# Optimization experiments

Hardware: AMD Instinct MI355X
Metric: run time of the kernel (lower is better)

The kernel has to match this reference:

```python
import jax, jax.numpy as jnp
import numpy as np

T = 64      # simulation_length
B = 128     # batch
D = 2048    # flattened input dim / axons per core
N = 2048    # neurons per core
L = 4       # number of cores (chain, latency = index)
OUT = 1024  # number of output_sources


def setup_inputs() -> dict:
    key = jax.random.key(0)
    k0, k1, k2, k3 = jax.random.split(key, 4)
    x = jax.random.uniform(k0, (B, D), dtype=jnp.float32)          # rate-coded input in [0,1)
    # core_params[l] = core_matrix.transpose() -> shape [N, A]; scaled for sane membrane dynamics
    W = jax.random.normal(k1, (L, N, D), dtype=jnp.float32) * 0.05
    thresholds = jnp.ones((L,), dtype=jnp.float32)
    # axon_sources: per-core irregular gather indices into previous core's neurons (input for l=0)
    axon_idx = jax.random.randint(k2, (L, D), 0, D, dtype=jnp.int32)
    out_idx = jax.random.randint(k3, (OUT,), 0, N, dtype=jnp.int32)
    return dict(x=x, W=W, thresholds=thresholds, axon_idx=axon_idx,
                out_idx=out_idx, simulation_length=T)


def _ideal_spike_scan(avg, thr, T):
    """Per-cycle: m += avg; spike = (m > thr); m[m > thr] -= thr.  avg: [B, N]."""
    def step(m, _):
        m = m + avg
        s = (m > thr).astype(m.dtype)
        return m - thr * s, s
    _, spikes = jax.lax.scan(step, jnp.zeros_like(avg), None, length=T)
    return spikes  # [T, B, N]


def reference(x, W, thresholds, axon_idx, out_idx, simulation_length):
    T = simulation_length
    L = W.shape[0]
    # generate_input_spike_train: x replicated across all cycles -> cache[-1]
    prev = jnp.broadcast_to(x, (T,) + x.shape)  # [T, B, D]
    for l in range(L):
        # get_signal_tensor: gather axon source signals for every cycle
        gathered = prev[:, :, axon_idx[l]]                    # [T, B, A]
        # per-cycle matmul: torch.matmul(core_params, sig.T).T == sig @ W[l].T
        val = jnp.einsum('tba,na->tbn', gathered, W[l])       # [T, B, N]
        avg = val.mean(axis=0)                                # avg_values [B, N]
        # ideal membrane integrate + threshold-reset recurrence -> out spike train
        prev = _ideal_spike_scan(avg, thresholds[l], T)       # [T, B, N]
    # output_signals: sum of output-source spikes over all cycles
    return prev[:, :, out_idx].sum(axis=0)                    # [B, OUT]
```

## Files before the change

kernel.cpp:

```cpp
#include <hip/hip_runtime.h>

#define BB   128
#define DD   2048
#define NN   2048
#define LL   4
#define OUTN 1024
#define JBQ  32
#define NDIG 5

#define NWDIG 12288
#define NG0   1024
#define NCSR  4

typedef double double4v __attribute__((ext_vector_type(4)));
typedef int    int4v    __attribute__((ext_vector_type(4)));
typedef char   char4v   __attribute__((ext_vector_type(4)));

__global__ __launch_bounds__(256) void prep_kernel(
    const float* __restrict__ W1,
    const float* __restrict__ x,
    const int*   __restrict__ axon,
    const int*   __restrict__ oidx,
    signed char* __restrict__ Wd,
    float*       __restrict__ At,
    int*         __restrict__ off,
    int*         __restrict__ lst)
{
    __shared__ int hist[2048];
    __shared__ int part[256];

    const int t  = threadIdx.x;
    const int bk = blockIdx.x;
    const size_t DP = (size_t)NN * DD;

    if (bk < NWDIG) {
        size_t i  = (size_t)bk * 256 + t;
        int    l  = (int)(i / (DP / 4));
        size_t e4 = i - (size_t)l * (DP / 4);
        int n = (int)(e4 >> 9);
        int k = (int)(e4 & 511) * 4;
        float4 w = *(const float4*)(W1 + (size_t)l * DP + (size_t)n * DD + k);
        const float wv[4] = {w.x, w.y, w.z, w.w};
        unsigned long long V[4];
        #pragma unroll
        for (int e = 0; e < 4; ++e)
            V[e] = (unsigned long long)(__double2ll_rn((double)wv[e] * 0x1p33)
                                        + (1LL << 34));
        signed char* base = Wd + (size_t)l * 5 * DP
                          + (size_t)(n >> 5) * 65536 + (size_t)(k >> 6) * 2048
                          + (n & 31) * 64 + (k & 63);
        #pragma unroll
        for (int j = 0; j < NDIG; ++j) {
            char4v p = { (char)((V[0] >> (7 * j)) & 127),
                         (char)((V[1] >> (7 * j)) & 127),
                         (char)((V[2] >> (7 * j)) & 127),
                         (char)((V[3] >> (7 * j)) & 127) };
            *(char4v*)(base + (size_t)j * DP) = p;
        }
        return;
    }
    if (bk < NWDIG + NG0) {
        int i = (bk - NWDIG) * 256 + t;
        int b = i >> 11;
        int k = i & (DD - 1);
        At[(size_t)(k >> 6) * 8192 + b * 64 + (k & 63)] = x[b * DD + axon[k]];
        return;
    }
    {
        const int m   = bk - (NWDIG + NG0);
        const int* ip = (m < 3) ? (axon + (size_t)(m + 1) * DD) : oidx;
        const int cnt = (m < 3) ? DD : OUTN;
        int* offG = off + m * 2052;
        int* lstG = lst + m * 2048;

        for (int i = t; i < 2048; i += 256) hist[i] = 0;
        __syncthreads();
        for (int e = t; e < cnt; e += 256) atomicAdd(&hist[ip[e]], 1);
        __syncthreads();

        const int b0 = t * 8;
        int s = 0;
        #pragma unroll
        for (int i = 0; i < 8; ++i) s += hist[b0 + i];
        part[t] = s;
        __syncthreads();
        for (int d = 1; d < 256; d <<= 1) {
            int v = (t >= d) ? part[t - d] : 0;
            __syncthreads();
            part[t] += v;
            __syncthreads();
        }
        int base = part[t] - s;
        #pragma unroll
        for (int i = 0; i < 8; ++i) {
            int h = hist[b0 + i];
            offG[b0 + i] = base;
            hist[b0 + i] = base;
            base += h;
        }
        if (t == 255) offG[2048] = base;
        __syncthreads();
        for (int e = t; e < cnt; e += 256) {
            int n = ip[e];
            int pos = atomicAdd(&hist[n], 1);
            lstG[pos] = e;
        }
    }
}

__global__ __launch_bounds__(256, 4) void layer0_kernel(
    const float* __restrict__ Atile,
    const float* __restrict__ Wl,
    const float* __restrict__ thr,
    const int*   __restrict__ Tptr,
    const int* __restrict__ goff, const int* __restrict__ glst,
    signed char* __restrict__ g8n)
{
    __shared__ double red[4 * 64 * 4];

    const int t    = threadIdx.x;
    const int wq   = t >> 6;
    const int lane = t & 63;
    const int q    = lane >> 4;
    const int c    = lane & 15;

    const int g     = blockIdx.x;
    const int btile = (g >> 3) & 7;
    const int nsup  = (g & 7) | ((g >> 6) << 3);
    const int n0    = nsup * 16;
    const int bcol  = btile * 16 + c;

    double4v pr = {0., 0., 0., 0.}, pcv = {0., 0., 0., 0.};
    pr  = __builtin_amdgcn_mfma_f64_16x16x4f64(0.25 * (double)c, 1.0, pr, 0, 0, 0);
    pcv = __builtin_amdgcn_mfma_f64_16x16x4f64(0.25, (double)c, pcv, 0, 0, 0);
    int rowD[4], colD[4];
    #pragma unroll
    for (int r = 0; r < 4; ++r) {
        rowD[r] = (int)(pr[r] + 0.25);
        colD[r] = (int)(pcv[r] + 0.25);
    }

    double4v acc[4] = {{0.,0.,0.,0.},{0.,0.,0.,0.},{0.,0.,0.,0.},{0.,0.,0.,0.}};

    const int    kbase = wq * (DD / 4);
    const float* wb0   = Wl + (size_t)(n0 + c) * DD + kbase + 4 * q;

    float4 wv0[4], sv[4];
    #pragma unroll
    for (int p = 0; p < 4; ++p) wv0[p] = *(const float4*)(wb0 + 16 * p);
    #pragma unroll
    for (int p = 0; p < 4; ++p) {
        int kabs = kbase + 16 * p + 4 * q;
        sv[p] = *(const float4*)(Atile + (size_t)(kabs >> 6) * 8192
                                 + bcol * 64 + (kabs & 63));
    }

    for (int u = 0; u < JBQ / 4; ++u) {
        #pragma unroll
        for (int gg = 0; gg < 4; ++gg) {
            float4 w0 = wv0[gg];
            float4 s  = sv[gg];

            int jn = 4 * u + 4 + gg; if (jn > JBQ - 1) jn = JBQ - 1;
            wv0[gg] = *(const float4*)(wb0 + 16 * jn);
            int kabs = kbase + 16 * jn + 4 * q;
            sv[gg] = *(const float4*)(Atile + (size_t)(kabs >> 6) * 8192
                                      + bcol * 64 + (kabs & 63));

            acc[0] = __builtin_amdgcn_mfma_f64_16x16x4f64((double)w0.x, (double)s.x, acc[0], 0, 0, 0);
            acc[1] = __builtin_amdgcn_mfma_f64_16x16x4f64((double)w0.y, (double)s.y, acc[1], 0, 0, 0);
            acc[2] = __builtin_amdgcn_mfma_f64_16x16x4f64((double)w0.z, (double)s.z, acc[2], 0, 0, 0);
            acc[3] = __builtin_amdgcn_mfma_f64_16x16x4f64((double)w0.w, (double)s.w, acc[3], 0, 0, 0);
        }
    }

    double4v a0 = (acc[0] + acc[1]) + (acc[2] + acc[3]);
    {
        double* my = red + ((size_t)wq * 64 + lane) * 4;
        #pragma unroll
        for (int r = 0; r < 4; ++r) my[r] = a0[r];
    }
    __syncthreads();
    if (wq == 0) {
        double a[4];
        #pragma unroll
        for (int r = 0; r < 4; ++r) {
            a[r] =  red[((size_t)0 * 64 + lane) * 4 + r];
            a[r] += red[((size_t)1 * 64 + lane) * 4 + r];
            a[r] += red[((size_t)2 * 64 + lane) * 4 + r];
            a[r] += red[((size_t)3 * 64 + lane) * 4 + r];
        }

        const double th = (double)thr[0];
        const int T = *Tptr;
        double m0 = 0., m1 = 0., m2 = 0., m3 = 0.;
        int c0 = 0, c1 = 0, c2 = 0, c3 = 0;
        for (int tt = 0; tt < T; ++tt) {
            m0 += a[0]; if (m0 > th) { c0++; m0 -= th; }
            m1 += a[1]; if (m1 > th) { c1++; m1 -= th; }
            m2 += a[2]; if (m2 > th) { c2++; m2 -= th; }
            m3 += a[3]; if (m3 > th) { c3++; m3 -= th; }
        }
        int cnt[4] = {c0, c1, c2, c3};
        #pragma unroll
        for (int r = 0; r < 4; ++r) {
            int n = n0 + rowD[r];
            int b = btile * 16 + colD[r];
            for (int j = goff[n]; j < goff[n + 1]; ++j) {
                int k = glst[j];
                g8n[(size_t)(k >> 6) * 8192 + b * 64 + (k & 63)] =
                    (signed char)cnt[r];
            }
        }
    }
}

__global__ __launch_bounds__(256, 4) void layer_i8_kernel(
    const signed char* __restrict__ B8,
    const signed char* __restrict__ Wd5,
    const float* __restrict__ thr, int l,
    const int*   __restrict__ Tptr,
    const int* __restrict__ goff, const int* __restrict__ glst,
    signed char* __restrict__ g8n,
    const int* __restrict__ ooff, const int* __restrict__ olst,
    float* __restrict__ outp)
{
    __shared__ double red[4 * 64 * 4];

    const int t    = threadIdx.x;
    const int wq   = t >> 6;
    const int lane = t & 63;
    const int q    = lane >> 4;
    const int c    = lane & 15;

    const int g     = blockIdx.x;
    const int btile = (g >> 3) & 7;
    const int nsup  = (g & 7) | ((g >> 6) << 3);
    const int n0    = nsup * 16;
    const int bcol  = btile * 16 + c;

    int rowD[4], colD[4];
    {
        const int cb  = c * 0x01010101;
        const int hot = (q == 0) ? 1 : 0;
        int4v aLab = {cb, cb, cb, cb};
        int4v oneh = {hot, 0, 0, 0};
        int4v dR = {0, 0, 0, 0}, dC = {0, 0, 0, 0};
        dR = __builtin_amdgcn_mfma_i32_16x16x64_i8(aLab, oneh, dR, 0, 0, 0);
        dC = __builtin_amdgcn_mfma_i32_16x16x64_i8(oneh, aLab, dC, 0, 0, 0);
        #pragma unroll
        for (int r = 0; r < 4; ++r) { rowD[r] = dR[r]; colD[r] = dC[r]; }
    }

    int4v acc[NDIG], accS = (int4v)0;
    #pragma unroll
    for (int j = 0; j < NDIG; ++j) acc[j] = (int4v)0;

    const size_t DP = (size_t)NN * DD;
    const signed char* ab = Wd5 + (size_t)(nsup >> 1) * 65536
                          + (nsup & 1) * 1024 + c * 64 + q * 16;
    const signed char* bb = B8 + bcol * 64 + q * 16;

    const int4v ones = {0x01010101, 0x01010101, 0x01010101, 0x01010101};
    const int ck0 = wq * 8;

    #pragma unroll 1
    for (int kc = 0; kc < 8; ++kc) {
        const signed char* ap = ab + (size_t)(ck0 + kc) * 2048;
        int4v A[NDIG], Bv;
        #pragma unroll
        for (int j = 0; j < NDIG; ++j)
            A[j] = *(const int4v*)(ap + (size_t)j * DP);
        Bv = *(const int4v*)(bb + (size_t)(ck0 + kc) * 8192);
        #pragma unroll
        for (int j = 0; j < NDIG; ++j)
            acc[j] = __builtin_amdgcn_mfma_i32_16x16x64_i8(A[j], Bv, acc[j], 0, 0, 0);
        accS = __builtin_amdgcn_mfma_i32_16x16x64_i8(ones, Bv, accS, 0, 0, 0);
    }

    const double S0 = 0x1p-33, S1 = 0x1p-26, S2 = 0x1p-19,
                 S3 = 0x1p-12, S4 = 0x1p-5;
    {
        double* my = red + ((size_t)wq * 64 + lane) * 4;
        #pragma unroll
        for (int r = 0; r < 4; ++r) {
            my[r] = S0 * (double)acc[0][r] + S1 * (double)acc[1][r]
                  + S2 * (double)acc[2][r] + S3 * (double)acc[3][r]
                  + S4 * (double)acc[4][r] - 2.0 * (double)accS[r];
        }
    }
    __syncthreads();
    if (wq == 0) {
        double a[4];
        #pragma unroll
        for (int r = 0; r < 4; ++r) {
            a[r] =  red[((size_t)0 * 64 + lane) * 4 + r];
            a[r] += red[((size_t)1 * 64 + lane) * 4 + r];
            a[r] += red[((size_t)2 * 64 + lane) * 4 + r];
            a[r] += red[((size_t)3 * 64 + lane) * 4 + r];
        }

        const double th = (double)thr[l];
        const int T = *Tptr;
        const double invT = 1.0 / (double)T;
        double m0 = 0., m1 = 0., m2 = 0., m3 = 0.;
        int c0 = 0, c1 = 0, c2 = 0, c3 = 0;
        const double v0 = a[0] * invT, v1 = a[1] * invT,
                     v2 = a[2] * invT, v3 = a[3] * invT;
        for (int tt = 0; tt < T; ++tt) {
            m0 += v0; if (m0 > th) { c0++; m0 -= th; }
            m1 += v1; if (m1 > th) { c1++; m1 -= th; }
            m2 += v2; if (m2 > th) { c2++; m2 -= th; }
            m3 += v3; if (m3 > th) { c3++; m3 -= th; }
        }
        int cnt[4] = {c0, c1, c2, c3};
        #pragma unroll
        for (int r = 0; r < 4; ++r) {
            int n = n0 + rowD[r];
            int b = btile * 16 + colD[r];
            if (goff) {
                for (int j = goff[n]; j < goff[n + 1]; ++j) {
                    int k = glst[j];
                    g8n[(size_t)(k >> 6) * 8192 + b * 64 + (k & 63)] =
                        (signed char)cnt[r];
                }
            }
            if (ooff) {
                for (int j = ooff[n]; j < ooff[n + 1]; ++j)
                    outp[(size_t)b * OUTN + olst[j]] = (float)cnt[r];
            }
        }
    }
}

__global__ __launch_bounds__(256, 2) void layer_kernel(
    const float* __restrict__ src,
    const int*   __restrict__ idx,
    int sR, int sB,
    const float* __restrict__ Wl,
    const float* __restrict__ thresholds, int l,
    const int*   __restrict__ Tptr,
    float* __restrict__ dst, int isLast)
{
    __shared__ double red[4 * 64 * 8];

    const int t    = threadIdx.x;
    const int wq   = t >> 6;
    const int lane = t & 63;
    const int q    = lane >> 4;
    const int c    = lane & 15;

    const int g     = blockIdx.x;
    const int btile = (g >> 3) & 7;
    const int nsup  = (g & 7) | ((g >> 6) << 3);
    const int n0    = nsup * 32;
    const int bcol  = btile * 16 + c;
    const size_t bo = (size_t)bcol * sB;

    double4v pr = {0., 0., 0., 0.}, pcv = {0., 0., 0., 0.};
    pr  = __builtin_amdgcn_mfma_f64_16x16x4f64(0.25 * (double)c, 1.0, pr, 0, 0, 0);
    pcv = __builtin_amdgcn_mfma_f64_16x16x4f64(0.25, (double)c, pcv, 0, 0, 0);
    int rowD[4], colD[4];
    #pragma unroll
    for (int r = 0; r < 4; ++r) {
        rowD[r] = (int)(pr[r] + 0.25);
        colD[r] = (int)(pcv[r] + 0.25);
    }

    double4v acc0[4] = {{0.,0.,0.,0.},{0.,0.,0.,0.},{0.,0.,0.,0.},{0.,0.,0.,0.}};
    double4v acc1[4] = {{0.,0.,0.,0.},{0.,0.,0.,0.},{0.,0.,0.,0.},{0.,0.,0.,0.}};

    const int    kbase = wq * (DD / 4);
    const float* wb0   = Wl + (size_t)(n0 + c) * DD + kbase + 4 * q;
    const float* wb1   = wb0 + (size_t)16 * DD;
    const int*   ibase = idx ? (idx + kbase + 4 * q) : nullptr;

    float4 wv0[4], wv1[4];
    float4 sv[4];
    int4   iv[4];

    #pragma unroll
    for (int p = 0; p < 4; ++p) {
        wv0[p] = *(const float4*)(wb0 + 16 * p);
        wv1[p] = *(const float4*)(wb1 + 16 * p);
    }
    #pragma unroll
    for (int p = 0; p < 4; ++p) {
        int r0, r1, r2, r3;
        if (ibase) {
            int4 iv0 = *(const int4*)(ibase + 16 * p);
            r0 = iv0.x; r1 = iv0.y; r2 = iv0.z; r3 = iv0.w;
        } else {
            int kb = kbase + 16 * p + 4 * q;
            r0 = kb; r1 = kb + 1; r2 = kb + 2; r3 = kb + 3;
        }
        sv[p].x = src[(size_t)r0 * sR + bo];
        sv[p].y = src[(size_t)r1 * sR + bo];
        sv[p].z = src[(size_t)r2 * sR + bo];
        sv[p].w = src[(size_t)r3 * sR + bo];
    }
    if (ibase) {
        #pragma unroll
        for (int p = 0; p < 4; ++p) iv[p] = *(const int4*)(ibase + 16 * (4 + p));
    }

    for (int u = 0; u < JBQ / 4; ++u) {
        #pragma unroll
        for (int gg = 0; gg < 4; ++gg) {
            float4 w0 = wv0[gg];
            float4 w1 = wv1[gg];
            float4 s  = sv[gg];

            int jn = 4 * u + 4 + gg; if (jn > JBQ - 1) jn = JBQ - 1;
            wv0[gg] = *(const float4*)(wb0 + 16 * jn);
            wv1[gg] = *(const float4*)(wb1 + 16 * jn);

            int r0, r1, r2, r3;
            if (ibase) {
                int4 ivv = iv[gg];
                r0 = ivv.x; r1 = ivv.y; r2 = ivv.z; r3 = ivv.w;
            } else {
                int kb = kbase + 16 * jn + 4 * q;
                r0 = kb; r1 = kb + 1; r2 = kb + 2; r3 = kb + 3;
            }
            sv[gg].x = src[(size_t)r0 * sR + bo];
            sv[gg].y = src[(size_t)r1 * sR + bo];
            sv[gg].z = src[(size_t)r2 * sR + bo];
            sv[gg].w = src[(size_t)r3 * sR + bo];

            if (ibase) {
                int jm = 4 * u + 8 + gg; if (jm > JBQ - 1) jm = JBQ - 1;
                iv[gg] = *(const int4*)(ibase + 16 * jm);
            }

            acc0[0] = __builtin_amdgcn_mfma_f64_16x16x4f64((double)w0.x, (double)s.x, acc0[0], 0, 0, 0);
            acc1[0] = __builtin_amdgcn_mfma_f64_16x16x4f64((double)w1.x, (double)s.x, acc1[0], 0, 0, 0);
            acc0[1] = __builtin_amdgcn_mfma_f64_16x16x4f64((double)w0.y, (double)s.y, acc0[1], 0, 0, 0);
            acc1[1] = __builtin_amdgcn_mfma_f64_16x16x4f64((double)w1.y, (double)s.y, acc1[1], 0, 0, 0);
            acc0[2] = __builtin_amdgcn_mfma_f64_16x16x4f64((double)w0.z, (double)s.z, acc0[2], 0, 0, 0);
            acc1[2] = __builtin_amdgcn_mfma_f64_16x16x4f64((double)w1.z, (double)s.z, acc1[2], 0, 0, 0);
            acc0[3] = __builtin_amdgcn_mfma_f64_16x16x4f64((double)w0.w, (double)s.w, acc0[3], 0, 0, 0);
            acc1[3] = __builtin_amdgcn_mfma_f64_16x16x4f64((double)w1.w, (double)s.w, acc1[3], 0, 0, 0);
        }
    }

    double4v a0 = (acc0[0] + acc0[1]) + (acc0[2] + acc0[3]);
    double4v a1 = (acc1[0] + acc1[1]) + (acc1[2] + acc1[3]);

    {
        double* my = red + ((size_t)wq * 64 + lane) * 8;
        #pragma unroll
        for (int r = 0; r < 4; ++r) { my[r] = a0[r]; my[4 + r] = a1[r]; }
    }
    __syncthreads();
    if (wq < 2) {
        const int off = wq * 4;
        double a[4];
        #pragma unroll
        for (int r = 0; r < 4; ++r) {
            a[r] =  red[((size_t)0 * 64 + lane) * 8 + off + r];
            a[r] += red[((size_t)1 * 64 + lane) * 8 + off + r];
            a[r] += red[((size_t)2 * 64 + lane) * 8 + off + r];
            a[r] += red[((size_t)3 * 64 + lane) * 8 + off + r];
        }

        const double th = (double)thresholds[l];
        const int T = *Tptr;
        const float sc = isLast ? 1.0f : (1.0f / (float)T);
        double m0 = 0., m1 = 0., m2 = 0., m3 = 0.;
        int c0 = 0, c1 = 0, c2 = 0, c3 = 0;
        for (int tt = 0; tt < T; ++tt) {
            m0 += a[0]; if (m0 > th) { c0++; m0 -= th; }
            m1 += a[1]; if (m1 > th) { c1++; m1 -= th; }
            m2 += a[2]; if (m2 > th) { c2++; m2 -= th; }
            m3 += a[3]; if (m3 > th) { c3++; m3 -= th; }
        }
        int cnt[4] = {c0, c1, c2, c3};
        #pragma unroll
        for (int r = 0; r < 4; ++r) {
            int n = n0 + 16 * wq + rowD[r];
            int b = btile * 16 + colD[r];
            dst[(size_t)n * BB + b] = (float)cnt[r] * sc;
        }
    }
}

__global__ __launch_bounds__(256) void out_kernel(
    const float* __restrict__ cntT, const int* __restrict__ out_idx,
    float* __restrict__ out)
{
    int i = blockIdx.x * 256 + threadIdx.x;
    int b = i >> 10;
    int o = i & 1023;
    out[i] = cntT[(size_t)out_idx[o] * BB + b];
}

extern "C" void kernel_launch(void* const* d_in, const int* in_sizes, int n_in,
                              void* d_out, int out_size, void* d_ws, size_t ws_size,
                              hipStream_t stream)
{
    const float* x    = (const float*)d_in[0];
    const float* W    = (const float*)d_in[1];
    const float* thr  = (const float*)d_in[2];
    const int*   axon = (const int*)d_in[3];
    const int*   oidx = (const int*)d_in[4];
    const int*   Tptr = (const int*)d_in[5];
    float* out = (float*)d_out;

    const size_t DP = (size_t)NN * DD;
    char* ws = (char*)d_ws;
    float* At   = (float*)ws;
    float* mA   = (float*)(ws + (1u << 20));
    float* mB   = (float*)(ws + (2u << 20));
    float* cntT = (float*)(ws + (3u << 20));
    signed char* g8A = (signed char*)(ws + (4u << 20));
    signed char* g8B = (signed char*)(ws + (4u << 20) + (256u << 10));
    int* off = (int*)(ws + (4u << 20) + (512u << 10));
    int* lst = (int*)(ws + (4u << 20) + (640u << 10));
    signed char* Wd  = (signed char*)(ws + (5u << 20));

    const int useI8 = (ws_size >= ((size_t)80 << 20)) ? 1 : 0;

    if (!useI8) {
        const float* srcs[LL] = { x, mA, mB, mA };
        float*       dsts[LL] = { mA, mB, mA, cntT };
        for (int l = 0; l < LL; ++l) {
            layer_kernel<<<512, 256, 0, stream>>>(
                srcs[l], axon + (size_t)l * DD,
                (l == 0) ? 1 : BB, (l == 0) ? DD : 1,
                W + (size_t)l * NN * DD, thr, l, Tptr,
                dsts[l], (l == LL - 1) ? 1 : 0);
        }
        out_kernel<<<(BB * OUTN) / 256, 256, 0, stream>>>(cntT, oidx, out);
        return;
    }

    prep_kernel<<<NWDIG + NG0 + NCSR, 256, 0, stream>>>(
        W + DP, x, axon, oidx, Wd, At, off, lst);

    layer0_kernel<<<1024, 256, 0, stream>>>(
        At, W, thr, Tptr, off + 0 * 2052, lst + 0 * 2048, g8A);

    layer_i8_kernel<<<1024, 256, 0, stream>>>(
        g8A, Wd + 0 * 5 * DP, thr, 1, Tptr,
        off + 1 * 2052, lst + 1 * 2048, g8B,
        nullptr, nullptr, nullptr);
    layer_i8_kernel<<<1024, 256, 0, stream>>>(
        g8B, Wd + 1 * 5 * DP, thr, 2, Tptr,
        off + 2 * 2052, lst + 2 * 2048, g8A,
        nullptr, nullptr, nullptr);
    layer_i8_kernel<<<1024, 256, 0, stream>>>(
        g8A, Wd + 2 * 5 * DP, thr, 3, Tptr,
        nullptr, nullptr, nullptr,
        off + 3 * 2052, lst + 3 * 2048, out);
}
```

Before: 218.2 us.

## Switch int8 layer GEMM to 32x32x32 MFMA with 32-wide tiles and 8 waves

Replaces the 16x16x64 int8 MFMA tiling with 32x32x32 MFMA over 32x32 output tiles. The weight-digit and spike-count layouts are re-blocked to 32-byte k-chunks, and the per-block K split goes from 4 to 8 waves in 512-thread blocks. The cross-wave reduction and the spike recurrence are now spread over all waves instead of one. The aim is higher MFMA throughput per operand load and less serial epilogue work, at the cost of fewer blocks (256), more accumulator registers and a larger shared-memory footprint.

```diff
diff --git a/kernel.cpp b/kernel.cpp
--- a/kernel.cpp
+++ b/kernel.cpp
@@ -14,7 +14,14 @@
 
 typedef double double4v __attribute__((ext_vector_type(4)));
 typedef int    int4v    __attribute__((ext_vector_type(4)));
+typedef int    int16v   __attribute__((ext_vector_type(16)));
 typedef char   char4v   __attribute__((ext_vector_type(4)));
+
+__device__ __forceinline__ size_t g8addr(int k, int b)
+{
+    return (size_t)(k >> 5) * 4096 + (size_t)(b >> 5) * 1024
+         + (b & 31) * 32 + (k & 31);
+}
 
 __global__ __launch_bounds__(256) void prep_kernel(
     const float* __restrict__ W1,
@@ -47,8 +54,8 @@
             V[e] = (unsigned long long)(__double2ll_rn((double)wv[e] * 0x1p33)
                                         + (1LL << 34));
         signed char* base = Wd + (size_t)l * 5 * DP
-                          + (size_t)(n >> 5) * 65536 + (size_t)(k >> 6) * 2048
-                          + (n & 31) * 64 + (k & 63);
+                          + (size_t)(n >> 5) * 65536 + (size_t)(k >> 5) * 1024
+                          + (n & 31) * 32 + (k & 31);
         #pragma unroll
         for (int j = 0; j < NDIG; ++j) {
             char4v p = { (char)((V[0] >> (7 * j)) & 127),
@@ -208,14 +215,13 @@
             int b = btile * 16 + colD[r];
             for (int j = goff[n]; j < goff[n + 1]; ++j) {
                 int k = glst[j];
-                g8n[(size_t)(k >> 6) * 8192 + b * 64 + (k & 63)] =
-                    (signed char)cnt[r];
+                g8n[g8addr(k, b)] = (signed char)cnt[r];
             }
         }
     }
 }
 
-__global__ __launch_bounds__(256, 4) void layer_i8_kernel(
+__global__ __launch_bounds__(512, 1) void layer_i8_kernel(
     const signed char* __restrict__ B8,
     const signed char* __restrict__ Wd5,
     const float* __restrict__ thr, int l,
@@ -225,109 +231,107 @@
     const int* __restrict__ ooff, const int* __restrict__ olst,
     float* __restrict__ outp)
 {
-    __shared__ double red[4 * 64 * 4];
+    __shared__ double red[8 * 64 * 16];
 
     const int t    = threadIdx.x;
     const int wq   = t >> 6;
     const int lane = t & 63;
-    const int q    = lane >> 4;
-    const int c    = lane & 15;
+    const int lr   = lane & 31;
+    const int lh   = lane >> 5;
 
     const int g     = blockIdx.x;
-    const int btile = (g >> 3) & 7;
-    const int nsup  = (g & 7) | ((g >> 6) << 3);
-    const int n0    = nsup * 16;
-    const int bcol  = btile * 16 + c;
-
-    int rowD[4], colD[4];
+    const int btile = g >> 6;
+    const int nsup  = g & 63;
+    const int n0    = nsup * 32;
+    const int b0    = btile * 32;
+
+    int16v acc[NDIG], accS = (int16v)0;
+    #pragma unroll
+    for (int j = 0; j < NDIG; ++j) acc[j] = (int16v)0;
+
+    const size_t DP = (size_t)NN * DD;
+    const signed char* ab = Wd5 + (size_t)nsup * 65536 + lr * 32 + lh * 16;
+    const signed char* bb = B8 + btile * 1024 + lr * 32 + lh * 16;
+
+    const int4v ones = {0x01010101, 0x01010101, 0x01010101, 0x01010101};
+    const int ck0 = wq * 8;
+
+    #pragma unroll 1
+    for (int kc = 0; kc < 8; ++kc) {
+        const signed char* ap = ab + (size_t)(ck0 + kc) * 1024;
+        int4v A[NDIG], Bv;
+        #pragma unroll
+        for (int j = 0; j < NDIG; ++j)
+            A[j] = *(const int4v*)(ap + (size_t)j * DP);
+        Bv = *(const int4v*)(bb + (size_t)(ck0 + kc) * 4096);
+        #pragma unroll
+        for (int j = 0; j < NDIG; ++j)
+            acc[j] = __builtin_amdgcn_mfma_i32_32x32x32_i8(A[j], Bv, acc[j], 0, 0, 0);
+        accS = __builtin_amdgcn_mfma_i32_32x32x32_i8(ones, Bv, accS, 0, 0, 0);
+    }
+
+    int rowD[16], colD[16];
     {
-        const int cb  = c * 0x01010101;
-        const int hot = (q == 0) ? 1 : 0;
+        const int cb  = lr * 0x01010101;
+        const int hot = (lane < 32) ? 1 : 0;
         int4v aLab = {cb, cb, cb, cb};
         int4v oneh = {hot, 0, 0, 0};
-        int4v dR = {0, 0, 0, 0}, dC = {0, 0, 0, 0};
-        dR = __builtin_amdgcn_mfma_i32_16x16x64_i8(aLab, oneh, dR, 0, 0, 0);
-        dC = __builtin_amdgcn_mfma_i32_16x16x64_i8(oneh, aLab, dC, 0, 0, 0);
-        #pragma unroll
-        for (int r = 0; r < 4; ++r) { rowD[r] = dR[r]; colD[r] = dC[r]; }
-    }
-
-    int4v acc[NDIG], accS = (int4v)0;
-    #pragma unroll
-    for (int j = 0; j < NDIG; ++j) acc[j] = (int4v)0;
-
-    const size_t DP = (size_t)NN * DD;
-    const signed char* ab = Wd5 + (size_t)(nsup >> 1) * 65536
-                          + (nsup & 1) * 1024 + c * 64 + q * 16;
-    const signed char* bb = B8 + bcol * 64 + q * 16;
-
-    const int4v ones = {0x01010101, 0x01010101, 0x01010101, 0x01010101};
-    const int ck0 = wq * 8;
-
-    #pragma unroll 1
-    for (int kc = 0; kc < 8; ++kc) {
-        const signed char* ap = ab + (size_t)(ck0 + kc) * 2048;
-        int4v A[NDIG], Bv;
-        #pragma unroll
-        for (int j = 0; j < NDIG; ++j)
-            A[j] = *(const int4v*)(ap + (size_t)j * DP);
-        Bv = *(const int4v*)(bb + (size_t)(ck0 + kc) * 8192);
-        #pragma unroll
-        for (int j = 0; j < NDIG; ++j)
-            acc[j] = __builtin_amdgcn_mfma_i32_16x16x64_i8(A[j], Bv, acc[j], 0, 0, 0);
-        accS = __builtin_amdgcn_mfma_i32_16x16x64_i8(ones, Bv, accS, 0, 0, 0);
+        int16v dR = (int16v)0, dC = (int16v)0;
+        dR = __builtin_amdgcn_mfma_i32_32x32x32_i8(aLab, oneh, dR, 0, 0, 0);
+        dC = __builtin_amdgcn_mfma_i32_32x32x32_i8(oneh, aLab, dC, 0, 0, 0);
+        #pragma unroll
+        for (int r = 0; r < 16; ++r) { rowD[r] = dR[r]; colD[r] = dC[r]; }
     }
 
     const double S0 = 0x1p-33, S1 = 0x1p-26, S2 = 0x1p-19,
                  S3 = 0x1p-12, S4 = 0x1p-5;
     {
-        double* my = red + ((size_t)wq * 64 + lane) * 4;
-        #pragma unroll
-        for (int r = 0; r < 4; ++r) {
+        double* my = red + ((size_t)wq * 64 + lane) * 16;
+        #pragma unroll
+        for (int r = 0; r < 16; ++r) {
             my[r] = S0 * (double)acc[0][r] + S1 * (double)acc[1][r]
                   + S2 * (double)acc[2][r] + S3 * (double)acc[3][r]
                   + S4 * (double)acc[4][r] - 2.0 * (double)accS[r];
         }
     }
     __syncthreads();
-    if (wq == 0) {
-        double a[4];
-        #pragma unroll
-        for (int r = 0; r < 4; ++r) {
-            a[r] =  red[((size_t)0 * 64 + lane) * 4 + r];
-            a[r] += red[((size_t)1 * 64 + lane) * 4 + r];
-            a[r] += red[((size_t)2 * 64 + lane) * 4 + r];
-            a[r] += red[((size_t)3 * 64 + lane) * 4 + r];
+    {
+        double a[2];
+        #pragma unroll
+        for (int r2 = 0; r2 < 2; ++r2) {
+            const int r = wq * 2 + r2;
+            double s = 0.;
+            #pragma unroll
+            for (int w = 0; w < 8; ++w)
+                s += red[((size_t)w * 64 + lane) * 16 + r];
+            a[r2] = s;
         }
 
         const double th = (double)thr[l];
         const int T = *Tptr;
         const double invT = 1.0 / (double)T;
-        double m0 = 0., m1 = 0., m2 = 0., m3 = 0.;
-        int c0 = 0, c1 = 0, c2 = 0, c3 = 0;
-        const double v0 = a[0] * invT, v1 = a[1] * invT,
-                     v2 = a[2] * invT, v3 = a[3] * invT;
+        double m0 = 0., m1 = 0.;
+        int c0 = 0, c1 = 0;
+        const double v0 = a[0] * invT, v1 = a[1] * invT;
         for (int tt = 0; tt < T; ++tt) {
             m0 += v0; if (m0 > th) { c0++; m0 -= th; }
             m1 += v1; if (m1 > th) { c1++; m1 -= th; }
-            m2 += v2; if (m2 > th) { c2++; m2 -= th; }
-            m3 += v3; if (m3 > th) { c3++; m3 -= th; }
-        }
-        int cnt[4] = {c0, c1, c2, c3};
-        #pragma unroll
-        for (int r = 0; r < 4; ++r) {
+        }
+        int cnt[2] = {c0, c1};
+        #pragma unroll
+        for (int r2 = 0; r2 < 2; ++r2) {
+            const int r = wq * 2 + r2;
             int n = n0 + rowD[r];
-            int b = btile * 16 + colD[r];
+            int b = b0 + colD[r];
             if (goff) {
                 for (int j = goff[n]; j < goff[n + 1]; ++j) {
                     int k = glst[j];
-                    g8n[(size_t)(k >> 6) * 8192 + b * 64 + (k & 63)] =
-                        (signed char)cnt[r];
+                    g8n[g8addr(k, b)] = (signed char)cnt[r2];
                 }
             }
             if (ooff) {
                 for (int j = ooff[n]; j < ooff[n + 1]; ++j)
-                    outp[(size_t)b * OUTN + olst[j]] = (float)cnt[r];
+                    outp[(size_t)b * OUTN + olst[j]] = (float)cnt[r2];
             }
         }
     }
@@ -541,15 +545,15 @@
     layer0_kernel<<<1024, 256, 0, stream>>>(
         At, W, thr, Tptr, off + 0 * 2052, lst + 0 * 2048, g8A);
 
-    layer_i8_kernel<<<1024, 256, 0, stream>>>(
+    layer_i8_kernel<<<256, 512, 0, stream>>>(
         g8A, Wd + 0 * 5 * DP, thr, 1, Tptr,
         off + 1 * 2052, lst + 1 * 2048, g8B,
         nullptr, nullptr, nullptr);
-    layer_i8_kernel<<<1024, 256, 0, stream>>>(
+    layer_i8_kernel<<<256, 512, 0, stream>>>(
         g8B, Wd + 1 * 5 * DP, thr, 2, Tptr,
         off + 2 * 2052, lst + 2 * 2048, g8A,
         nullptr, nullptr, nullptr);
-    layer_i8_kernel<<<1024, 256, 0, stream>>>(
+    layer_i8_kernel<<<256, 512, 0, stream>>>(
         g8A, Wd + 2 * 5 * DP, thr, 3, Tptr,
         nullptr, nullptr, nullptr,
         off + 3 * 2052, lst + 3 * 2048, out);
```

Measured after the change: 231.7 us. 1.06x slower.
